# Kernel optimization log

Measured on AMD Instinct MI355X. Metric: run time of the kernel, lower is better.

Reference implementation:

```python
import jax, jax.numpy as jnp
import numpy as np

B, S, H = 8, 2048, 1024
D = H // 16  # head_size = hidden_size // n_heads = 64


def setup_inputs() -> dict:
    key = jax.random.key(0)
    ks = jax.random.split(key, 7)
    scale = 1.0 / np.sqrt(H)
    x = jax.random.normal(ks[0], (B, S, H), dtype=jnp.float32)
    mask = jnp.ones((B, S), dtype=jnp.int32)
    Wq = jax.random.uniform(ks[1], (H, D), jnp.float32, -scale, scale)
    bq = jax.random.uniform(ks[2], (D,), jnp.float32, -scale, scale)
    Wk = jax.random.uniform(ks[3], (H, D), jnp.float32, -scale, scale)
    bk = jax.random.uniform(ks[4], (D,), jnp.float32, -scale, scale)
    Wv = jax.random.uniform(ks[5], (H, D), jnp.float32, -scale, scale)
    bv = jax.random.uniform(ks[6], (D,), jnp.float32, -scale, scale)
    return {"x": x, "mask": mask, "Wq": Wq, "bq": bq, "Wk": Wk, "bk": bk, "Wv": Wv, "bv": bv}


def reference(x, mask, Wq, bq, Wk, bk, Wv, bv):
    # projections: [B,S,H] @ [H,D] -> [B,S,D]
    q = jnp.einsum("bsh,hd->bsd", x, Wq) + bq
    k = jnp.einsum("bsh,hd->bsd", x, Wk) + bk
    v = jnp.einsum("bsh,hd->bsd", x, Wv) + bv
    # scores: [B,S,S]
    scores = jnp.einsum("bqd,bkd->bqk", q, k) / jnp.sqrt(jnp.asarray(q.shape[-1], q.dtype))
    # mask: [B,S] -> [B,1,S]; fill masked keys with -inf
    scores = jnp.where(mask[:, None, :] == 0, -jnp.inf, scores)
    attn = jax.nn.softmax(scores, axis=-1)
    # dropout prob is 0.0 (inference semantics) -> identity
    return jnp.einsum("bqk,bkd->bqd", attn, v)
```

## Files before the change

### kernel.cpp

```cpp
#include <hip/hip_runtime.h>

typedef __bf16 bf16x8 __attribute__((ext_vector_type(8)));
typedef __bf16 bf16x4 __attribute__((ext_vector_type(4)));
typedef float f32x4 __attribute__((ext_vector_type(4)));
typedef unsigned short u16x8 __attribute__((ext_vector_type(8)));

#define MFMA16(a, b, c) __builtin_amdgcn_mfma_f32_16x16x32_bf16((a), (b), (c), 0, 0, 0)

static __device__ __forceinline__ unsigned short f2bf(float f) {
  unsigned int u = __float_as_uint(f);
  u += 0x7fffu + ((u >> 16) & 1u);
  return (unsigned short)(u >> 16);
}
static __device__ __forceinline__ float bf2f(unsigned short s) {
  return __uint_as_float((unsigned int)s << 16);
}

static __device__ __forceinline__ void gld_lds16(const void* g, void* l) {
  __builtin_amdgcn_global_load_lds(
      (const __attribute__((address_space(1))) unsigned int*)(g),
      (__attribute__((address_space(3))) unsigned int*)(l), 16, 0, 0);
}

__global__ __launch_bounds__(128) void wt_kernel(
    const float* __restrict__ Wq, const float* __restrict__ Wk,
    const float* __restrict__ Wv, unsigned short* __restrict__ Wt,
    const int* __restrict__ mask, float* __restrict__ mAddG) {
  const int bid = blockIdx.x;
  if (bid >= 192) {
    const int idx = (bid - 192) * 128 + threadIdx.x;
    mAddG[idx] = mask[idx] ? 0.0f : -__builtin_inff();
    return;
  }
  const int n = bid;
  const int jl = threadIdx.x;
  const float* W;
  int col;
  float scale;
  if (n < 64)       { W = Wq; col = n;       scale = 0.125f; }
  else if (n < 128) { W = Wk; col = n - 64;  scale = 1.0f; }
  else              { W = Wv; col = n - 128; scale = 1.0f; }
  const int js = (jl & ~7) | ((jl & 7) ^ (n & 7));
  u16x8 o;
#pragma unroll
  for (int e = 0; e < 8; ++e) o[e] = f2bf(W[(jl * 8 + e) * 64 + col] * scale);
  *reinterpret_cast<u16x8*>(&Wt[n * 1024 + js * 8]) = o;
}

__global__ __launch_bounds__(512, 4) void qkv_kernel(
    const float* __restrict__ x, const unsigned short* __restrict__ Wt,
    const float* __restrict__ bq, const float* __restrict__ bk,
    const float* __restrict__ bv, unsigned short* __restrict__ Q,
    unsigned short* __restrict__ K, unsigned short* __restrict__ Vt) {
  __shared__ __align__(16) unsigned short xs[2][32][72];
  __shared__ __align__(16) unsigned short ws[2][192 * 64];
  const int tid = threadIdx.x;
  const int w = tid >> 6, lane = tid & 63;
  const int lr = lane & 15, lg = lane >> 4;
  const int wg = w >> 2, wc = w & 3;
  const int m0 = blockIdx.x * 32;

  const int xrow = tid >> 4, xc4 = (tid & 15) * 4;
  const float* xsrc = x + (m0 + xrow) * 1024 + xc4;
  const unsigned short* wsrc0 = Wt + ((0 * 512 + tid) >> 3) * 1024 + (tid & 7) * 8;
  const unsigned short* wsrc1 = Wt + ((1 * 512 + tid) >> 3) * 1024 + (tid & 7) * 8;
  const unsigned short* wsrc2 = Wt + ((2 * 512 + tid) >> 3) * 1024 + (tid & 7) * 8;

  f32x4 acc[3] = {};
  const int arow = wg * 16 + lr;

#define WSTAGE(k0, buf)                                                      \
  do {                                                                       \
    gld_lds16(wsrc0 + (k0), (char*)(&ws[buf][0]) + w * 1024);                \
    gld_lds16(wsrc1 + (k0), (char*)(&ws[buf][0]) + 8192 + w * 1024);         \
    gld_lds16(wsrc2 + (k0), (char*)(&ws[buf][0]) + 16384 + w * 1024);        \
  } while (0)
#define XWRITE(v, buf)                                                       \
  do {                                                                       \
    bf16x4 xb;                                                               \
    xb[0] = (__bf16)(v).x; xb[1] = (__bf16)(v).y;                            \
    xb[2] = (__bf16)(v).z; xb[3] = (__bf16)(v).w;                            \
    *reinterpret_cast<bf16x4*>(&xs[buf][xrow][xc4]) = xb;                    \
  } while (0)

  float4 xrA = *reinterpret_cast<const float4*>(xsrc);
  WSTAGE(0, 0);
  XWRITE(xrA, 0);
  xrA = *reinterpret_cast<const float4*>(xsrc + 64);
  asm volatile("s_waitcnt vmcnt(1) lgkmcnt(0)" ::: "memory");
  __builtin_amdgcn_s_barrier();

#pragma unroll
  for (int t = 0; t < 16; ++t) {
    const int cur = t & 1;
    if (t < 15) WSTAGE((t + 1) * 64, cur ^ 1);
    __builtin_amdgcn_sched_barrier(0);
    float4 xrB = {};
    if (t < 14)
      xrB = *reinterpret_cast<const float4*>(xsrc + (t + 2) * 64);
    __builtin_amdgcn_sched_barrier(0);

    bf16x8 a[2];
#pragma unroll
    for (int kh = 0; kh < 2; ++kh)
      a[kh] = *reinterpret_cast<const bf16x8*>(&xs[cur][arow][kh * 32 + lg * 8]);
#pragma unroll
    for (int cf = 0; cf < 3; ++cf) {
      const int n = wc * 48 + cf * 16 + lr;
      const unsigned short* wr = &ws[cur][n * 64];
#pragma unroll
      for (int kh = 0; kh < 2; ++kh) {
        const int sc = (kh * 4 + lg) ^ (n & 7);
        bf16x8 bv8 = *reinterpret_cast<const bf16x8*>(wr + sc * 8);
        acc[cf] = MFMA16(a[kh], bv8, acc[cf]);
      }
    }
    if (t < 15) {
      XWRITE(xrA, cur ^ 1);
      if (t < 14)
        asm volatile("s_waitcnt vmcnt(1) lgkmcnt(0)" ::: "memory");
      else
        asm volatile("s_waitcnt vmcnt(0) lgkmcnt(0)" ::: "memory");
      __builtin_amdgcn_s_barrier();
      xrA = xrB;
    }
  }
#undef WSTAGE
#undef XWRITE

  const int mb = m0 + wg * 16 + lg * 4;
  const int b = m0 >> 11;
#pragma unroll
  for (int cf = 0; cf < 3; ++cf) {
    const int n = wc * 48 + cf * 16 + lr;
    if (n < 64) {
      const float bias = bq[n] * 0.125f;
#pragma unroll
      for (int i = 0; i < 4; ++i) Q[(mb + i) * 64 + n] = f2bf(acc[cf][i] + bias);
    } else if (n < 128) {
      const int nn = n - 64;
      const float bias = bk[nn];
#pragma unroll
      for (int i = 0; i < 4; ++i) K[(mb + i) * 64 + nn] = f2bf(acc[cf][i] + bias);
    } else {
      const int d = n - 128;
      const float bias = bv[d];
      ushort4 o;
      o.x = f2bf(acc[cf][0] + bias);
      o.y = f2bf(acc[cf][1] + bias);
      o.z = f2bf(acc[cf][2] + bias);
      o.w = f2bf(acc[cf][3] + bias);
      const int sl = (m0 & 2047) + wg * 16 + lg * 4;
      *reinterpret_cast<ushort4*>(&Vt[((b * 64 + d) << 11) + sl]) = o;
    }
  }
}

__global__ __launch_bounds__(256, 4) void attn_kernel(
    const unsigned short* __restrict__ Q, const unsigned short* __restrict__ K,
    const unsigned short* __restrict__ Vt, const float* __restrict__ mAddG,
    unsigned short* __restrict__ Opb, float* __restrict__ mp,
    float* __restrict__ lp) {
  __shared__ __align__(16) unsigned short ks[64][72];
  __shared__ __align__(16) unsigned short vs[64][72];
  __shared__ __align__(16) unsigned short ps[4][32][72];

  const int b = blockIdx.y, c = blockIdx.z;
  const int tid = threadIdx.x;
  const int w = tid >> 6, lane = tid & 63;
  const int lr = lane & 15, lg = lane >> 4;
  const int bh = b * 2048;
  const int qb = blockIdx.x * 128 + w * 32;
  const int sr = tid >> 3, scc = (tid & 7) * 8;

  bf16x8 qf[2][2];
#pragma unroll
  for (int s = 0; s < 2; ++s)
#pragma unroll
    for (int kh = 0; kh < 2; ++kh)
      qf[s][kh] = *reinterpret_cast<const bf16x8*>(
          &Q[(bh + qb + s * 16 + lr) * 64 + kh * 32 + lg * 8]);

  bf16x8 vones;
#pragma unroll
  for (int j = 0; j < 8; ++j) vones[j] = (__bf16)1.0f;

  uint4 rk0, rk1, rv0, rv1;
  {
    const int kv0 = c * 256;
    rk0 = *reinterpret_cast<const uint4*>(&K[(bh + kv0 + sr) * 64 + scc]);
    rk1 = *reinterpret_cast<const uint4*>(&K[(bh + kv0 + 32 + sr) * 64 + scc]);
    rv0 = *reinterpret_cast<const uint4*>(&Vt[(b * 64 + sr) * 2048 + kv0 + scc]);
    rv1 = *reinterpret_cast<const uint4*>(&Vt[(b * 64 + 32 + sr) * 2048 + kv0 + scc]);
  }

  f32x4 oacc[2][4] = {};
  f32x4 lacc[2] = {};
  float m_s[2];
#pragma unroll
  for (int s = 0; s < 2; ++s) m_s[s] = -__builtin_inff();

  for (int it = 0; it < 4; ++it) {
    const int kv0 = c * 256 + it * 64;
    __builtin_amdgcn_s_barrier();

    f32x4 mdc[4];
#pragma unroll
    for (int f = 0; f < 4; ++f)
      mdc[f] = *reinterpret_cast<const f32x4*>(&mAddG[bh + kv0 + f * 16 + lg * 4]);

    *reinterpret_cast<uint4*>(&ks[sr][scc]) = rk0;
    *reinterpret_cast<uint4*>(&ks[32 + sr][scc]) = rk1;
    *reinterpret_cast<uint4*>(&vs[sr][scc]) = rv0;
    *reinterpret_cast<uint4*>(&vs[32 + sr][scc]) = rv1;

    if (it < 3) {
      const int kvn = kv0 + 64;
      rk0 = *reinterpret_cast<const uint4*>(&K[(bh + kvn + sr) * 64 + scc]);
      rk1 = *reinterpret_cast<const uint4*>(&K[(bh + kvn + 32 + sr) * 64 + scc]);
      rv0 = *reinterpret_cast<const uint4*>(&Vt[(b * 64 + sr) * 2048 + kvn + scc]);
      rv1 = *reinterpret_cast<const uint4*>(&Vt[(b * 64 + 32 + sr) * 2048 + kvn + scc]);
    }

    asm volatile("s_waitcnt lgkmcnt(0)" ::: "memory");
    __builtin_amdgcn_s_barrier();

    f32x4 st[2][4];
    __builtin_amdgcn_s_setprio(1);
#pragma unroll
    for (int f = 0; f < 4; ++f) {
      const bf16x8 kf0 = *reinterpret_cast<const bf16x8*>(&ks[f * 16 + lr][lg * 8]);
      const bf16x8 kf1 = *reinterpret_cast<const bf16x8*>(&ks[f * 16 + lr][32 + lg * 8]);
#pragma unroll
      for (int s = 0; s < 2; ++s) {
        f32x4 z = {};
        z = MFMA16(kf0, qf[s][0], z);
        z = MFMA16(kf1, qf[s][1], z);
        st[s][f] = z + mdc[f];
      }
    }
    __builtin_amdgcn_s_setprio(0);

#pragma unroll
    for (int s = 0; s < 2; ++s) {
      float pm = st[s][0][0];
#pragma unroll
      for (int f = 0; f < 4; ++f)
#pragma unroll
        for (int i = 0; i < 4; ++i) pm = fmaxf(pm, st[s][f][i]);
      pm = fmaxf(pm, __shfl_xor(pm, 16));
      pm = fmaxf(pm, __shfl_xor(pm, 32));
      const float nm = fmaxf(m_s[s], pm);
      if (!__all(nm <= m_s[s] + 8.0f)) {
        const float scn = __expf(m_s[s] - nm);
        m_s[s] = nm;
        float scb[4];
#pragma unroll
        for (int i = 0; i < 4; ++i) scb[i] = __shfl(scn, lg * 4 + i);
#pragma unroll
        for (int nf = 0; nf < 4; ++nf)
#pragma unroll
          for (int i = 0; i < 4; ++i) oacc[s][nf][i] *= scb[i];
#pragma unroll
        for (int i = 0; i < 4; ++i) lacc[s][i] *= scb[i];
      }
      const float mexp = (m_s[s] == -__builtin_inff()) ? 0.0f : m_s[s];
#pragma unroll
      for (int f = 0; f < 4; ++f) {
        bf16x4 pk;
#pragma unroll
        for (int i = 0; i < 4; ++i) {
          const float p = __expf(st[s][f][i] - mexp);
          pk[i] = (__bf16)p;
        }
        *reinterpret_cast<bf16x4*>(&ps[w][s * 16 + lr][f * 16 + lg * 4]) = pk;
      }
    }

    bf16x8 pa[2][2];
#pragma unroll
    for (int s = 0; s < 2; ++s)
#pragma unroll
      for (int k2 = 0; k2 < 2; ++k2)
        pa[s][k2] = *reinterpret_cast<const bf16x8*>(
            &ps[w][s * 16 + lr][k2 * 32 + lg * 8]);
    __builtin_amdgcn_s_setprio(1);
#pragma unroll
    for (int nf = 0; nf < 4; ++nf)
#pragma unroll
      for (int k2 = 0; k2 < 2; ++k2) {
        const bf16x8 vb = *reinterpret_cast<const bf16x8*>(
            &vs[nf * 16 + lr][k2 * 32 + lg * 8]);
#pragma unroll
        for (int s = 0; s < 2; ++s)
          oacc[s][nf] = MFMA16(pa[s][k2], vb, oacc[s][nf]);
      }
#pragma unroll
    for (int s = 0; s < 2; ++s)
#pragma unroll
      for (int k2 = 0; k2 < 2; ++k2)
        lacc[s] = MFMA16(pa[s][k2], vones, lacc[s]);
    __builtin_amdgcn_s_setprio(0);
  }

#pragma unroll
  for (int s = 0; s < 2; ++s) {
    float inv[4];
#pragma unroll
    for (int i = 0; i < 4; ++i)
      inv[i] = (lacc[s][i] > 0.0f) ? 1.0f / lacc[s][i] : 0.0f;
#pragma unroll
    for (int nf = 0; nf < 4; ++nf) {
      const int d = nf * 16 + lr;
#pragma unroll
      for (int i = 0; i < 4; ++i) {
        const int row = bh + qb + s * 16 + lg * 4 + i;
        Opb[(c * 16384 + row) * 64 + d] = f2bf(oacc[s][nf][i] * inv[i]);
      }
    }
    if (lg == 0) {
      const int r = c * 16384 + bh + qb + s * 16 + lr;
      mp[r] = m_s[s];
    }
    if (lr == 0) {
#pragma unroll
      for (int i = 0; i < 4; ++i)
        lp[c * 16384 + bh + qb + s * 16 + lg * 4 + i] = lacc[s][i];
    }
  }
}

__global__ __launch_bounds__(256) void merge_kernel(
    const unsigned short* __restrict__ Opb, const float* __restrict__ mp,
    const float* __restrict__ lp, float* __restrict__ out) {
  const int t = blockIdx.x * 256 + threadIdx.x;
  const int row = t >> 4;
  const int cc = (t & 15) * 4;
  float mv[8], lv[8];
#pragma unroll
  for (int c = 0; c < 8; ++c) {
    mv[c] = mp[c * 16384 + row];
    lv[c] = lp[c * 16384 + row];
  }
  float M = mv[0];
#pragma unroll
  for (int c = 1; c < 8; ++c) M = fmaxf(M, mv[c]);
  float L = 0.0f;
  f32x4 o = {};
#pragma unroll
  for (int c = 0; c < 8; ++c) {
    const float wc = __expf(mv[c] - M) * lv[c];
    L += wc;
    const ushort4 u = *reinterpret_cast<const ushort4*>(
        &Opb[(c * 16384 + row) * 64 + cc]);
    f32x4 oc;
    oc[0] = bf2f(u.x); oc[1] = bf2f(u.y); oc[2] = bf2f(u.z); oc[3] = bf2f(u.w);
    o += oc * wc;
  }
  const float inv = 1.0f / L;
  *reinterpret_cast<f32x4*>(&out[row * 64 + cc]) = o * inv;
}

extern "C" void kernel_launch(void* const* d_in, const int* in_sizes, int n_in,
                              void* d_out, int out_size, void* d_ws, size_t ws_size,
                              hipStream_t stream) {
  const float* x  = (const float*)d_in[0];
  const int* mask = (const int*)d_in[1];
  const float* Wq = (const float*)d_in[2];
  const float* bq = (const float*)d_in[3];
  const float* Wk = (const float*)d_in[4];
  const float* bk = (const float*)d_in[5];
  const float* Wv = (const float*)d_in[6];
  const float* bv = (const float*)d_in[7];
  float* out = (float*)d_out;

  unsigned short* Wt = (unsigned short*)d_ws;
  unsigned short* Qw = Wt + 192 * 1024;
  unsigned short* Kw = Qw + 16384 * 64;
  unsigned short* Vt = Kw + 16384 * 64;
  unsigned short* Opb = Vt + 16384 * 64;
  float* mAddG = (float*)(Opb + 8 * 16384 * 64);
  float* mp = mAddG + 16384;
  float* lp = mp + 8 * 16384;

  hipLaunchKernelGGL(wt_kernel, dim3(320), dim3(128), 0, stream,
                     Wq, Wk, Wv, Wt, mask, mAddG);
  hipLaunchKernelGGL(qkv_kernel, dim3(512), dim3(512), 0, stream,
                     x, Wt, bq, bk, bv, Qw, Kw, Vt);
  hipLaunchKernelGGL(attn_kernel, dim3(16, 8, 8), dim3(256), 0, stream,
                     Qw, Kw, Vt, mAddG, Opb, mp, lp);
  hipLaunchKernelGGL(merge_kernel, dim3(1024), dim3(256), 0, stream,
                     Opb, mp, lp, out);
}
```

Measured before the change: 57.39 us.

## Load x directly into MFMA registers and remap attention grid to 1D

The QKV projection stops staging x through shared memory. Each lane now loads its own fp32 A-fragment straight from global memory, converts it to bf16 in registers, and double-buffers it across k-steps. This removes the LDS write/read round trip and frees shared memory, and the occupancy hint rises from 4 to 6 blocks per SM. The attention launch is flattened to a 1D grid with batch as the fastest-varying index, which changes block scheduling order and L2 locality. The risks are redundant global reads of x, since the four column waves of each row group load the same rows, and higher register pressure.

```diff
diff --git a/kernel.cpp b/kernel.cpp
--- a/kernel.cpp
+++ b/kernel.cpp
@@ -47,12 +47,11 @@
   *reinterpret_cast<u16x8*>(&Wt[n * 1024 + js * 8]) = o;
 }
 
-__global__ __launch_bounds__(512, 4) void qkv_kernel(
+__global__ __launch_bounds__(512, 6) void qkv_kernel(
     const float* __restrict__ x, const unsigned short* __restrict__ Wt,
     const float* __restrict__ bq, const float* __restrict__ bk,
     const float* __restrict__ bv, unsigned short* __restrict__ Q,
     unsigned short* __restrict__ K, unsigned short* __restrict__ Vt) {
-  __shared__ __align__(16) unsigned short xs[2][32][72];
   __shared__ __align__(16) unsigned short ws[2][192 * 64];
   const int tid = threadIdx.x;
   const int w = tid >> 6, lane = tid & 63;
@@ -60,14 +59,13 @@
   const int wg = w >> 2, wc = w & 3;
   const int m0 = blockIdx.x * 32;
 
-  const int xrow = tid >> 4, xc4 = (tid & 15) * 4;
-  const float* xsrc = x + (m0 + xrow) * 1024 + xc4;
   const unsigned short* wsrc0 = Wt + ((0 * 512 + tid) >> 3) * 1024 + (tid & 7) * 8;
   const unsigned short* wsrc1 = Wt + ((1 * 512 + tid) >> 3) * 1024 + (tid & 7) * 8;
   const unsigned short* wsrc2 = Wt + ((2 * 512 + tid) >> 3) * 1024 + (tid & 7) * 8;
 
+  const float* asrc = x + (m0 + wg * 16 + lr) * 1024 + lg * 8;
+
   f32x4 acc[3] = {};
-  const int arow = wg * 16 + lr;
 
 #define WSTAGE(k0, buf)                                                      \
   do {                                                                       \
@@ -75,19 +73,19 @@
     gld_lds16(wsrc1 + (k0), (char*)(&ws[buf][0]) + 8192 + w * 1024);         \
     gld_lds16(wsrc2 + (k0), (char*)(&ws[buf][0]) + 16384 + w * 1024);        \
   } while (0)
-#define XWRITE(v, buf)                                                       \
+#define ALOAD(dst, k0)                                                       \
   do {                                                                       \
-    bf16x4 xb;                                                               \
-    xb[0] = (__bf16)(v).x; xb[1] = (__bf16)(v).y;                            \
-    xb[2] = (__bf16)(v).z; xb[3] = (__bf16)(v).w;                            \
-    *reinterpret_cast<bf16x4*>(&xs[buf][xrow][xc4]) = xb;                    \
+    _Pragma("unroll") for (int kh = 0; kh < 2; ++kh) {                       \
+      (dst)[kh][0] = *reinterpret_cast<const float4*>(asrc + (k0) + kh * 32);\
+      (dst)[kh][1] =                                                         \
+          *reinterpret_cast<const float4*>(asrc + (k0) + kh * 32 + 4);       \
+    }                                                                        \
   } while (0)
 
-  float4 xrA = *reinterpret_cast<const float4*>(xsrc);
+  float4 aA[2][2], aB[2][2];
   WSTAGE(0, 0);
-  XWRITE(xrA, 0);
-  xrA = *reinterpret_cast<const float4*>(xsrc + 64);
-  asm volatile("s_waitcnt vmcnt(1) lgkmcnt(0)" ::: "memory");
+  ALOAD(aA, 0);
+  asm volatile("s_waitcnt vmcnt(4)" ::: "memory");
   __builtin_amdgcn_s_barrier();
 
 #pragma unroll
@@ -95,15 +93,20 @@
     const int cur = t & 1;
     if (t < 15) WSTAGE((t + 1) * 64, cur ^ 1);
     __builtin_amdgcn_sched_barrier(0);
-    float4 xrB = {};
-    if (t < 14)
-      xrB = *reinterpret_cast<const float4*>(xsrc + (t + 2) * 64);
+    if (t < 15) ALOAD(aB, (t + 1) * 64);
     __builtin_amdgcn_sched_barrier(0);
 
     bf16x8 a[2];
 #pragma unroll
-    for (int kh = 0; kh < 2; ++kh)
-      a[kh] = *reinterpret_cast<const bf16x8*>(&xs[cur][arow][kh * 32 + lg * 8]);
+    for (int kh = 0; kh < 2; ++kh) {
+      union { u16x8 u; bf16x8 b; } cv;
+#pragma unroll
+      for (int j = 0; j < 4; ++j) {
+        cv.u[j] = f2bf(aA[kh][0][j]);
+        cv.u[4 + j] = f2bf(aA[kh][1][j]);
+      }
+      a[kh] = cv.b;
+    }
 #pragma unroll
     for (int cf = 0; cf < 3; ++cf) {
       const int n = wc * 48 + cf * 16 + lr;
@@ -116,17 +119,17 @@
       }
     }
     if (t < 15) {
-      XWRITE(xrA, cur ^ 1);
-      if (t < 14)
-        asm volatile("s_waitcnt vmcnt(1) lgkmcnt(0)" ::: "memory");
-      else
-        asm volatile("s_waitcnt vmcnt(0) lgkmcnt(0)" ::: "memory");
+      asm volatile("s_waitcnt vmcnt(4) lgkmcnt(0)" ::: "memory");
       __builtin_amdgcn_s_barrier();
-      xrA = xrB;
+#pragma unroll
+      for (int kh = 0; kh < 2; ++kh) {
+        aA[kh][0] = aB[kh][0];
+        aA[kh][1] = aB[kh][1];
+      }
     }
   }
 #undef WSTAGE
-#undef XWRITE
+#undef ALOAD
 
   const int mb = m0 + wg * 16 + lg * 4;
   const int b = m0 >> 11;
@@ -165,12 +168,15 @@
   __shared__ __align__(16) unsigned short vs[64][72];
   __shared__ __align__(16) unsigned short ps[4][32][72];
 
-  const int b = blockIdx.y, c = blockIdx.z;
+  const int id = blockIdx.x;
+  const int b = id & 7;
+  const int rest = id >> 3;
+  const int qt = rest & 15, c = rest >> 4;
   const int tid = threadIdx.x;
   const int w = tid >> 6, lane = tid & 63;
   const int lr = lane & 15, lg = lane >> 4;
   const int bh = b * 2048;
-  const int qb = blockIdx.x * 128 + w * 32;
+  const int qb = qt * 128 + w * 32;
   const int sr = tid >> 3, scc = (tid & 7) * 8;
 
   bf16x8 qf[2][2];
@@ -387,7 +393,7 @@
                      Wq, Wk, Wv, Wt, mask, mAddG);
   hipLaunchKernelGGL(qkv_kernel, dim3(512), dim3(512), 0, stream,
                      x, Wt, bq, bk, bv, Qw, Kw, Vt);
-  hipLaunchKernelGGL(attn_kernel, dim3(16, 8, 8), dim3(256), 0, stream,
+  hipLaunchKernelGGL(attn_kernel, dim3(1024), dim3(256), 0, stream,
                      Qw, Kw, Vt, mAddG, Opb, mp, lp);
   hipLaunchKernelGGL(merge_kernel, dim3(1024), dim3(256), 0, stream,
                      Opb, mp, lp, out);
```

Result: slower. 80.41 us (+40.1%).

## Switch attention to 32x32 MFMA with register-resident P and fewer KV splits

Applied to the files above, without the earlier changes.

Rewrites the attention kernel to use 32x32x16 bf16 MFMA tiles. The softmax probabilities are packed into bf16 in registers via cvt_pk and permlane32_swap, which removes the per-wave LDS staging buffer and the ones-vector MFMA previously used to compute row sums. Row sums are now computed with scalar adds plus a cross-half shuffle. The KV split count is halved from 8 to 4, so each block runs 8 iterations, the merge reads 4 partials and less workspace is used. The tradeoffs are fewer blocks (512) available to fill the GPU, and the occupancy hint is dropped from the launch bounds.

```diff
diff --git a/kernel.cpp b/kernel.cpp
--- a/kernel.cpp
+++ b/kernel.cpp
@@ -3,9 +3,11 @@
 typedef __bf16 bf16x8 __attribute__((ext_vector_type(8)));
 typedef __bf16 bf16x4 __attribute__((ext_vector_type(4)));
 typedef float f32x4 __attribute__((ext_vector_type(4)));
+typedef float f32x16 __attribute__((ext_vector_type(16)));
 typedef unsigned short u16x8 __attribute__((ext_vector_type(8)));
 
 #define MFMA16(a, b, c) __builtin_amdgcn_mfma_f32_16x16x32_bf16((a), (b), (c), 0, 0, 0)
+#define MFMA32(a, b, c) __builtin_amdgcn_mfma_f32_32x32x16_bf16((a), (b), (c), 0, 0, 0)
 
 static __device__ __forceinline__ unsigned short f2bf(float f) {
   unsigned int u = __float_as_uint(f);
@@ -14,6 +16,14 @@
 }
 static __device__ __forceinline__ float bf2f(unsigned short s) {
   return __uint_as_float((unsigned int)s << 16);
+}
+static __device__ __forceinline__ unsigned int cvtpk(float lo, float hi) {
+  unsigned int r;
+  asm("v_cvt_pk_bf16_f32 %0, %1, %2" : "=v"(r) : "v"(lo), "v"(hi));
+  return r;
+}
+static __device__ __forceinline__ void plswap(unsigned int& a, unsigned int& b) {
+  asm("v_permlane32_swap_b32 %0, %1" : "+v"(a), "+v"(b));
 }
 
 static __device__ __forceinline__ void gld_lds16(const void* g, void* l) {
@@ -156,65 +166,57 @@
   }
 }
 
-__global__ __launch_bounds__(256, 4) void attn_kernel(
+__global__ __launch_bounds__(256) void attn_kernel(
     const unsigned short* __restrict__ Q, const unsigned short* __restrict__ K,
     const unsigned short* __restrict__ Vt, const float* __restrict__ mAddG,
     unsigned short* __restrict__ Opb, float* __restrict__ mp,
     float* __restrict__ lp) {
   __shared__ __align__(16) unsigned short ks[64][72];
   __shared__ __align__(16) unsigned short vs[64][72];
-  __shared__ __align__(16) unsigned short ps[4][32][72];
-
-  const int b = blockIdx.y, c = blockIdx.z;
+
+  const int qt = blockIdx.x, b = blockIdx.y, c = blockIdx.z;
   const int tid = threadIdx.x;
   const int w = tid >> 6, lane = tid & 63;
-  const int lr = lane & 15, lg = lane >> 4;
+  const int l31 = lane & 31, h = lane >> 5;
   const int bh = b * 2048;
-  const int qb = blockIdx.x * 128 + w * 32;
+  const int qb = qt * 128 + w * 32;
   const int sr = tid >> 3, scc = (tid & 7) * 8;
 
-  bf16x8 qf[2][2];
-#pragma unroll
-  for (int s = 0; s < 2; ++s)
-#pragma unroll
-    for (int kh = 0; kh < 2; ++kh)
-      qf[s][kh] = *reinterpret_cast<const bf16x8*>(
-          &Q[(bh + qb + s * 16 + lr) * 64 + kh * 32 + lg * 8]);
-
-  bf16x8 vones;
-#pragma unroll
-  for (int j = 0; j < 8; ++j) vones[j] = (__bf16)1.0f;
+  bf16x8 qf[4];
+#pragma unroll
+  for (int dt = 0; dt < 4; ++dt)
+    qf[dt] = *reinterpret_cast<const bf16x8*>(
+        &Q[(bh + qb + l31) * 64 + dt * 16 + h * 8]);
 
   uint4 rk0, rk1, rv0, rv1;
   {
-    const int kv0 = c * 256;
+    const int kv0 = c * 512;
     rk0 = *reinterpret_cast<const uint4*>(&K[(bh + kv0 + sr) * 64 + scc]);
     rk1 = *reinterpret_cast<const uint4*>(&K[(bh + kv0 + 32 + sr) * 64 + scc]);
     rv0 = *reinterpret_cast<const uint4*>(&Vt[(b * 64 + sr) * 2048 + kv0 + scc]);
     rv1 = *reinterpret_cast<const uint4*>(&Vt[(b * 64 + 32 + sr) * 2048 + kv0 + scc]);
   }
 
-  f32x4 oacc[2][4] = {};
-  f32x4 lacc[2] = {};
-  float m_s[2];
-#pragma unroll
-  for (int s = 0; s < 2; ++s) m_s[s] = -__builtin_inff();
-
-  for (int it = 0; it < 4; ++it) {
-    const int kv0 = c * 256 + it * 64;
+  f32x16 oacc[2] = {};
+  float m_s = -__builtin_inff(), l_s = 0.0f;
+
+  for (int it = 0; it < 8; ++it) {
+    const int kv0 = c * 512 + it * 64;
     __builtin_amdgcn_s_barrier();
 
-    f32x4 mdc[4];
-#pragma unroll
-    for (int f = 0; f < 4; ++f)
-      mdc[f] = *reinterpret_cast<const f32x4*>(&mAddG[bh + kv0 + f * 16 + lg * 4]);
+    f32x4 md0[4], md1[4];
+#pragma unroll
+    for (int rb = 0; rb < 4; ++rb) {
+      md0[rb] = *reinterpret_cast<const f32x4*>(&mAddG[bh + kv0 + rb * 8 + 4 * h]);
+      md1[rb] = *reinterpret_cast<const f32x4*>(&mAddG[bh + kv0 + 32 + rb * 8 + 4 * h]);
+    }
 
     *reinterpret_cast<uint4*>(&ks[sr][scc]) = rk0;
     *reinterpret_cast<uint4*>(&ks[32 + sr][scc]) = rk1;
     *reinterpret_cast<uint4*>(&vs[sr][scc]) = rv0;
     *reinterpret_cast<uint4*>(&vs[32 + sr][scc]) = rv1;
 
-    if (it < 3) {
+    if (it < 7) {
       const int kvn = kv0 + 64;
       rk0 = *reinterpret_cast<const uint4*>(&K[(bh + kvn + sr) * 64 + scc]);
       rk1 = *reinterpret_cast<const uint4*>(&K[(bh + kvn + 32 + sr) * 64 + scc]);
@@ -225,108 +227,109 @@
     asm volatile("s_waitcnt lgkmcnt(0)" ::: "memory");
     __builtin_amdgcn_s_barrier();
 
-    f32x4 st[2][4];
+    f32x16 st0 = {}, st1 = {};
     __builtin_amdgcn_s_setprio(1);
 #pragma unroll
-    for (int f = 0; f < 4; ++f) {
-      const bf16x8 kf0 = *reinterpret_cast<const bf16x8*>(&ks[f * 16 + lr][lg * 8]);
-      const bf16x8 kf1 = *reinterpret_cast<const bf16x8*>(&ks[f * 16 + lr][32 + lg * 8]);
-#pragma unroll
-      for (int s = 0; s < 2; ++s) {
-        f32x4 z = {};
-        z = MFMA16(kf0, qf[s][0], z);
-        z = MFMA16(kf1, qf[s][1], z);
-        st[s][f] = z + mdc[f];
-      }
+    for (int dt = 0; dt < 4; ++dt) {
+      const bf16x8 kf0 = *reinterpret_cast<const bf16x8*>(&ks[l31][dt * 16 + h * 8]);
+      st0 = MFMA32(kf0, qf[dt], st0);
+    }
+#pragma unroll
+    for (int dt = 0; dt < 4; ++dt) {
+      const bf16x8 kf1 = *reinterpret_cast<const bf16x8*>(&ks[32 + l31][dt * 16 + h * 8]);
+      st1 = MFMA32(kf1, qf[dt], st1);
     }
     __builtin_amdgcn_s_setprio(0);
 
 #pragma unroll
-    for (int s = 0; s < 2; ++s) {
-      float pm = st[s][0][0];
-#pragma unroll
-      for (int f = 0; f < 4; ++f)
-#pragma unroll
-        for (int i = 0; i < 4; ++i) pm = fmaxf(pm, st[s][f][i]);
-      pm = fmaxf(pm, __shfl_xor(pm, 16));
-      pm = fmaxf(pm, __shfl_xor(pm, 32));
-      const float nm = fmaxf(m_s[s], pm);
-      if (!__all(nm <= m_s[s] + 8.0f)) {
-        const float scn = __expf(m_s[s] - nm);
-        m_s[s] = nm;
-        float scb[4];
-#pragma unroll
-        for (int i = 0; i < 4; ++i) scb[i] = __shfl(scn, lg * 4 + i);
-#pragma unroll
-        for (int nf = 0; nf < 4; ++nf)
-#pragma unroll
-          for (int i = 0; i < 4; ++i) oacc[s][nf][i] *= scb[i];
-#pragma unroll
-        for (int i = 0; i < 4; ++i) lacc[s][i] *= scb[i];
-      }
-      const float mexp = (m_s[s] == -__builtin_inff()) ? 0.0f : m_s[s];
-#pragma unroll
-      for (int f = 0; f < 4; ++f) {
-        bf16x4 pk;
-#pragma unroll
-        for (int i = 0; i < 4; ++i) {
-          const float p = __expf(st[s][f][i] - mexp);
-          pk[i] = (__bf16)p;
-        }
-        *reinterpret_cast<bf16x4*>(&ps[w][s * 16 + lr][f * 16 + lg * 4]) = pk;
-      }
-    }
-
-    bf16x8 pa[2][2];
-#pragma unroll
-    for (int s = 0; s < 2; ++s)
-#pragma unroll
-      for (int k2 = 0; k2 < 2; ++k2)
-        pa[s][k2] = *reinterpret_cast<const bf16x8*>(
-            &ps[w][s * 16 + lr][k2 * 32 + lg * 8]);
+    for (int rb = 0; rb < 4; ++rb)
+#pragma unroll
+      for (int j = 0; j < 4; ++j) {
+        st0[rb * 4 + j] += md0[rb][j];
+        st1[rb * 4 + j] += md1[rb][j];
+      }
+
+    float pm = st0[0];
+#pragma unroll
+    for (int r = 1; r < 16; ++r) pm = fmaxf(pm, st0[r]);
+#pragma unroll
+    for (int r = 0; r < 16; ++r) pm = fmaxf(pm, st1[r]);
+    pm = fmaxf(pm, __shfl_xor(pm, 32));
+    const float nm = fmaxf(m_s, pm);
+    if (!__all(nm <= m_s + 8.0f)) {
+      const float scn = __expf(m_s - nm);
+      m_s = nm;
+      l_s *= scn;
+#pragma unroll
+      for (int r = 0; r < 16; ++r) {
+        const float scr = __shfl(scn, (r & 3) + 8 * (r >> 2) + 4 * h);
+        oacc[0][r] *= scr;
+        oacc[1][r] *= scr;
+      }
+    }
+    const float mexp = (m_s == -__builtin_inff()) ? 0.0f : m_s;
+    float rs = 0.0f;
+#pragma unroll
+    for (int r = 0; r < 16; ++r) {
+      const float p0 = __expf(st0[r] - mexp);
+      st0[r] = p0;
+      rs += p0;
+      const float p1 = __expf(st1[r] - mexp);
+      st1[r] = p1;
+      rs += p1;
+    }
+    rs += __shfl_xor(rs, 32);
+    l_s += rs;
+
+    unsigned int paw[4][4];
+#pragma unroll
+    for (int kt16 = 0; kt16 < 4; ++kt16) {
+      const int lo = kt16 & 1;
+      unsigned int X0, X1, Y0, Y1;
+      if (kt16 < 2) {
+        X0 = cvtpk(st0[lo * 8 + 0], st0[lo * 8 + 1]);
+        Y0 = cvtpk(st0[lo * 8 + 2], st0[lo * 8 + 3]);
+        X1 = cvtpk(st0[lo * 8 + 4], st0[lo * 8 + 5]);
+        Y1 = cvtpk(st0[lo * 8 + 6], st0[lo * 8 + 7]);
+      } else {
+        X0 = cvtpk(st1[lo * 8 + 0], st1[lo * 8 + 1]);
+        Y0 = cvtpk(st1[lo * 8 + 2], st1[lo * 8 + 3]);
+        X1 = cvtpk(st1[lo * 8 + 4], st1[lo * 8 + 5]);
+        Y1 = cvtpk(st1[lo * 8 + 6], st1[lo * 8 + 7]);
+      }
+      plswap(X0, X1);
+      plswap(Y0, Y1);
+      paw[kt16][0] = X0;
+      paw[kt16][1] = Y0;
+      paw[kt16][2] = X1;
+      paw[kt16][3] = Y1;
+    }
+
     __builtin_amdgcn_s_setprio(1);
 #pragma unroll
-    for (int nf = 0; nf < 4; ++nf)
-#pragma unroll
-      for (int k2 = 0; k2 < 2; ++k2) {
+    for (int nf = 0; nf < 2; ++nf)
+#pragma unroll
+      for (int kt16 = 0; kt16 < 4; ++kt16) {
         const bf16x8 vb = *reinterpret_cast<const bf16x8*>(
-            &vs[nf * 16 + lr][k2 * 32 + lg * 8]);
-#pragma unroll
-        for (int s = 0; s < 2; ++s)
-          oacc[s][nf] = MFMA16(pa[s][k2], vb, oacc[s][nf]);
-      }
-#pragma unroll
-    for (int s = 0; s < 2; ++s)
-#pragma unroll
-      for (int k2 = 0; k2 < 2; ++k2)
-        lacc[s] = MFMA16(pa[s][k2], vones, lacc[s]);
+            &vs[nf * 32 + l31][kt16 * 16 + h * 8]);
+        const bf16x8 pa = *reinterpret_cast<const bf16x8*>(&paw[kt16][0]);
+        oacc[nf] = MFMA32(pa, vb, oacc[nf]);
+      }
     __builtin_amdgcn_s_setprio(0);
   }
 
-#pragma unroll
-  for (int s = 0; s < 2; ++s) {
-    float inv[4];
-#pragma unroll
-    for (int i = 0; i < 4; ++i)
-      inv[i] = (lacc[s][i] > 0.0f) ? 1.0f / lacc[s][i] : 0.0f;
-#pragma unroll
-    for (int nf = 0; nf < 4; ++nf) {
-      const int d = nf * 16 + lr;
-#pragma unroll
-      for (int i = 0; i < 4; ++i) {
-        const int row = bh + qb + s * 16 + lg * 4 + i;
-        Opb[(c * 16384 + row) * 64 + d] = f2bf(oacc[s][nf][i] * inv[i]);
-      }
-    }
-    if (lg == 0) {
-      const int r = c * 16384 + bh + qb + s * 16 + lr;
-      mp[r] = m_s[s];
-    }
-    if (lr == 0) {
-#pragma unroll
-      for (int i = 0; i < 4; ++i)
-        lp[c * 16384 + bh + qb + s * 16 + lg * 4 + i] = lacc[s][i];
-    }
+  const float inv_s = (l_s > 0.0f) ? 1.0f / l_s : 0.0f;
+#pragma unroll
+  for (int r = 0; r < 16; ++r) {
+    const int qoff = (r & 3) + 8 * (r >> 2) + 4 * h;
+    const float invr = __shfl(inv_s, qoff);
+    const int row = bh + qb + qoff;
+    Opb[(c * 16384 + row) * 64 + l31] = f2bf(oacc[0][r] * invr);
+    Opb[(c * 16384 + row) * 64 + 32 + l31] = f2bf(oacc[1][r] * invr);
+  }
+  if (h == 0) {
+    mp[c * 16384 + bh + qb + l31] = m_s;
+    lp[c * 16384 + bh + qb + l31] = l_s;
   }
 }
 
@@ -336,19 +339,17 @@
   const int t = blockIdx.x * 256 + threadIdx.x;
   const int row = t >> 4;
   const int cc = (t & 15) * 4;
-  float mv[8], lv[8];
-#pragma unroll
-  for (int c = 0; c < 8; ++c) {
+  float mv[4], lv[4];
+#pragma unroll
+  for (int c = 0; c < 4; ++c) {
     mv[c] = mp[c * 16384 + row];
     lv[c] = lp[c * 16384 + row];
   }
-  float M = mv[0];
-#pragma unroll
-  for (int c = 1; c < 8; ++c) M = fmaxf(M, mv[c]);
+  float M = fmaxf(fmaxf(mv[0], mv[1]), fmaxf(mv[2], mv[3]));
   float L = 0.0f;
   f32x4 o = {};
 #pragma unroll
-  for (int c = 0; c < 8; ++c) {
+  for (int c = 0; c < 4; ++c) {
     const float wc = __expf(mv[c] - M) * lv[c];
     L += wc;
     const ushort4 u = *reinterpret_cast<const ushort4*>(
@@ -379,15 +380,15 @@
   unsigned short* Kw = Qw + 16384 * 64;
   unsigned short* Vt = Kw + 16384 * 64;
   unsigned short* Opb = Vt + 16384 * 64;
-  float* mAddG = (float*)(Opb + 8 * 16384 * 64);
+  float* mAddG = (float*)(Opb + 4 * 16384 * 64);
   float* mp = mAddG + 16384;
-  float* lp = mp + 8 * 16384;
+  float* lp = mp + 4 * 16384;
 
   hipLaunchKernelGGL(wt_kernel, dim3(320), dim3(128), 0, stream,
                      Wq, Wk, Wv, Wt, mask, mAddG);
   hipLaunchKernelGGL(qkv_kernel, dim3(512), dim3(512), 0, stream,
                      x, Wt, bq, bk, bv, Qw, Kw, Vt);
-  hipLaunchKernelGGL(attn_kernel, dim3(16, 8, 8), dim3(256), 0, stream,
+  hipLaunchKernelGGL(attn_kernel, dim3(16, 8, 4), dim3(256), 0, stream,
                      Qw, Kw, Vt, mAddG, Opb, mp, lp);
   hipLaunchKernelGGL(merge_kernel, dim3(1024), dim3(256), 0, stream,
                      Opb, mp, lp, out);
```

Result: faster. 49.33 us (-14.0%).
